# Kernel tuning notes

Measured on AMD Instinct MI355X. Metric: run time of the kernel, lower is better.

The kernel has to match this reference:

```python
import jax, jax.numpy as jnp
import numpy as np

N = 50000
E = 800000
D_IN = 128
H = 256
L = 3


def setup_inputs() -> dict:
    key = jax.random.key(0)
    ks = jax.random.split(key, 12)
    x = jax.random.normal(ks[0], (N, D_IN), dtype=jnp.float32)
    edge_index = jax.random.randint(ks[1], (2, E), 0, N, dtype=jnp.int32)
    edge_attr = jax.random.uniform(ks[2], (E, 4), dtype=jnp.float32)
    s_enc = 1.0 / np.sqrt(D_IN)
    s_h = 1.0 / np.sqrt(H)
    W_enc = jax.random.uniform(ks[3], (D_IN, H), minval=-s_enc, maxval=s_enc)
    b_enc = jax.random.uniform(ks[4], (H,), minval=-s_enc, maxval=s_enc)
    W_g = jax.random.uniform(ks[5], (L, H, H), minval=-s_h, maxval=s_h)
    b_g = jax.random.uniform(ks[6], (L, H), minval=-s_h, maxval=s_h)
    W_out = jax.random.uniform(ks[7], (H, H), minval=-s_h, maxval=s_h)
    b_out = jax.random.uniform(ks[8], (H,), minval=-s_h, maxval=s_h)
    return {"x": x, "edge_index": edge_index, "edge_attr": edge_attr,
            "W_enc": W_enc, "b_enc": b_enc, "W_g": W_g, "b_g": b_g,
            "W_out": W_out, "b_out": b_out}


def _gcn_norm(edge_index, n):
    # PyG GCNConv: add self-loops, symmetric normalization D^-1/2 (A+I) D^-1/2
    loops = jnp.arange(n, dtype=edge_index.dtype)
    src = jnp.concatenate([edge_index[0], loops])  # [E+N]
    dst = jnp.concatenate([edge_index[1], loops])  # [E+N]
    deg = jax.ops.segment_sum(jnp.ones_like(dst, dtype=jnp.float32), dst, num_segments=n)
    dinv = jnp.where(deg > 0, jax.lax.rsqrt(deg), 0.0)
    norm = dinv[src] * dinv[dst]  # [E+N]
    return src, dst, norm


def _gcn_conv(h, W, b, src, dst, norm, n):
    m = h @ W                                  # [N,H] transform first
    agg = jax.ops.segment_sum(m[src] * norm[:, None], dst, num_segments=n)
    return agg + b


def reference(x, edge_index, edge_attr, W_enc, b_enc, W_g, b_g, W_out, b_out):
    n = x.shape[0]
    src, dst, norm = _gcn_norm(edge_index, n)
    h = jax.nn.relu(x @ W_enc + b_enc)
    for i in range(W_g.shape[0]):
        h = jax.nn.relu(_gcn_conv(h, W_g[i], b_g[i], src, dst, norm, n))
        # dropout is identity in eval mode
    return h @ W_out + b_out
```

## Files before the change

### kernel.cpp

```cpp
#include <hip/hip_runtime.h>
#include <math.h>

#define N_NODES 50000
#define N_EDGES 800000
#define D_IN    128
#define H_DIM   256
#define L_LAYERS 3
#define SCAN_BLOCKS ((N_NODES + 255) / 256)

typedef _Float16 f16x8 __attribute__((ext_vector_type(8)));
typedef _Float16 f16x4 __attribute__((ext_vector_type(4)));
typedef float    f32x4 __attribute__((ext_vector_type(4)));


__global__ __launch_bounds__(256) void zero_kernel(int* __restrict__ counts,
                                                   int* __restrict__ cursor, int n) {
    int i = blockIdx.x * 256 + threadIdx.x;
    if (i < n) { counts[i] = 0; cursor[i] = 0; }
}

__global__ __launch_bounds__(256) void hist_kernel(const int* __restrict__ dst,
                                                   int* __restrict__ counts, int e_cnt) {
    int e = blockIdx.x * 256 + threadIdx.x;
    if (e < e_cnt) atomicAdd(&counts[dst[e]], 1);
}

__global__ __launch_bounds__(256) void scanA_kernel(const int* __restrict__ counts,
                                                    int* __restrict__ blocksum,
                                                    float* __restrict__ dinv, int n) {
    __shared__ int s[256];
    int t = threadIdx.x;
    int i = blockIdx.x * 256 + t;
    int v = (i < n) ? counts[i] : 0;
    if (i < n) dinv[i] = rsqrtf((float)(v + 1));
    s[t] = v;
    __syncthreads();
#pragma unroll
    for (int d = 128; d > 0; d >>= 1) {
        if (t < d) s[t] += s[t + d];
        __syncthreads();
    }
    if (t == 0) blocksum[blockIdx.x] = s[0];
}

__global__ __launch_bounds__(256) void scanB_kernel(int* __restrict__ blocksum,
                                                    int* __restrict__ offsets,
                                                    int nblocks, int n, int total) {
    __shared__ int s[256];
    int t = threadIdx.x;
    int v = (t < nblocks) ? blocksum[t] : 0;
    s[t] = v;
    __syncthreads();
#pragma unroll
    for (int d = 1; d < 256; d <<= 1) {
        int x = (t >= d) ? s[t - d] : 0;
        __syncthreads();
        s[t] += x;
        __syncthreads();
    }
    if (t < nblocks) blocksum[t] = s[t] - v;
    if (t == 0) offsets[n] = total;
}

__global__ __launch_bounds__(256) void scanC_kernel(const int* __restrict__ counts,
                                                    const int* __restrict__ blocksum,
                                                    int* __restrict__ offsets, int n) {
    __shared__ int s[256];
    int t = threadIdx.x;
    int i = blockIdx.x * 256 + t;
    int v = (i < n) ? counts[i] : 0;
    s[t] = v;
    __syncthreads();
#pragma unroll
    for (int d = 1; d < 256; d <<= 1) {
        int x = (t >= d) ? s[t - d] : 0;
        __syncthreads();
        s[t] += x;
        __syncthreads();
    }
    if (i < n) offsets[i] = blocksum[blockIdx.x] + s[t] - v;
}

__global__ __launch_bounds__(256) void fill_kernel(const int* __restrict__ src,
                                                   const int* __restrict__ dst,
                                                   const int* __restrict__ offsets,
                                                   int* __restrict__ cursor,
                                                   const float* __restrict__ dinv,
                                                   int* __restrict__ csr_src,
                                                   float* __restrict__ csr_w, int e_cnt) {
    int e = blockIdx.x * 256 + threadIdx.x;
    if (e < e_cnt) {
        int d = dst[e];
        int pos = offsets[d] + atomicAdd(&cursor[d], 1);
        int s = src[e];
        csr_src[pos] = s;
        csr_w[pos]   = dinv[s];
    }
}


__global__ __launch_bounds__(256) void aggregate_kernel(const _Float16* __restrict__ h,
                                                        const int* __restrict__ offsets,
                                                        const int* __restrict__ csr_src,
                                                        const float* __restrict__ csr_w,
                                                        const float* __restrict__ dinv,
                                                        _Float16* __restrict__ outp, int n) {
    int wave = threadIdx.x >> 6;
    int lane = threadIdx.x & 63;
    int v = blockIdx.x * 4 + wave;
    if (v >= n) return;
    int c = lane * 4;
    float dv = dinv[v];
    f16x4 self = *(const f16x4*)(h + (size_t)v * H_DIM + c);
    float ax = dv * (float)self[0];
    float ay = dv * (float)self[1];
    float az = dv * (float)self[2];
    float aw = dv * (float)self[3];

    int e  = offsets[v];
    int e1 = offsets[v + 1];

    for (; e + 15 < e1; e += 16) {
        int   s_[16]; float w_[16]; f16x4 r_[16];
#pragma unroll
        for (int j = 0; j < 16; ++j) { s_[j] = csr_src[e + j]; w_[j] = csr_w[e + j]; }
#pragma unroll
        for (int j = 0; j < 16; ++j) r_[j] = *(const f16x4*)(h + (size_t)s_[j] * H_DIM + c);
#pragma unroll
        for (int j = 0; j < 16; ++j) {
            ax += w_[j] * (float)r_[j][0];
            ay += w_[j] * (float)r_[j][1];
            az += w_[j] * (float)r_[j][2];
            aw += w_[j] * (float)r_[j][3];
        }
    }
    if (e + 7 < e1) {
        int   s_[8]; float w_[8]; f16x4 r_[8];
#pragma unroll
        for (int j = 0; j < 8; ++j) { s_[j] = csr_src[e + j]; w_[j] = csr_w[e + j]; }
#pragma unroll
        for (int j = 0; j < 8; ++j) r_[j] = *(const f16x4*)(h + (size_t)s_[j] * H_DIM + c);
#pragma unroll
        for (int j = 0; j < 8; ++j) {
            ax += w_[j] * (float)r_[j][0];
            ay += w_[j] * (float)r_[j][1];
            az += w_[j] * (float)r_[j][2];
            aw += w_[j] * (float)r_[j][3];
        }
        e += 8;
    }
    if (e + 3 < e1) {
        int   s_[4]; float w_[4]; f16x4 r_[4];
#pragma unroll
        for (int j = 0; j < 4; ++j) { s_[j] = csr_src[e + j]; w_[j] = csr_w[e + j]; }
#pragma unroll
        for (int j = 0; j < 4; ++j) r_[j] = *(const f16x4*)(h + (size_t)s_[j] * H_DIM + c);
#pragma unroll
        for (int j = 0; j < 4; ++j) {
            ax += w_[j] * (float)r_[j][0];
            ay += w_[j] * (float)r_[j][1];
            az += w_[j] * (float)r_[j][2];
            aw += w_[j] * (float)r_[j][3];
        }
        e += 4;
    }
    if (e + 1 < e1) {
        int   s0 = csr_src[e],  s1 = csr_src[e + 1];
        float w0 = csr_w[e],    w1 = csr_w[e + 1];
        f16x4 a = *(const f16x4*)(h + (size_t)s0 * H_DIM + c);
        f16x4 b = *(const f16x4*)(h + (size_t)s1 * H_DIM + c);
        ax += w0 * (float)a[0] + w1 * (float)b[0];
        ay += w0 * (float)a[1] + w1 * (float)b[1];
        az += w0 * (float)a[2] + w1 * (float)b[2];
        aw += w0 * (float)a[3] + w1 * (float)b[3];
        e += 2;
    }
    if (e < e1) {
        int   s0 = csr_src[e];
        float w0 = csr_w[e];
        f16x4 a = *(const f16x4*)(h + (size_t)s0 * H_DIM + c);
        ax += w0 * (float)a[0]; ay += w0 * (float)a[1];
        az += w0 * (float)a[2]; aw += w0 * (float)a[3];
    }
    f16x4 o;
    o[0] = (_Float16)(ax * dv);
    o[1] = (_Float16)(ay * dv);
    o[2] = (_Float16)(az * dv);
    o[3] = (_Float16)(aw * dv);
    *(f16x4*)(outp + (size_t)v * H_DIM + c) = o;
}


#define WCONV_TOTAL 294912

__global__ __launch_bounds__(256) void wconv_kernel(const float* __restrict__ W_enc,
                                                    const float* __restrict__ W_g,
                                                    const float* __restrict__ W_out,
                                                    _Float16* __restrict__ whi,
                                                    _Float16* __restrict__ wlo) {
    int gid = blockIdx.x * 256 + threadIdx.x;
    if (gid >= WCONV_TOTAL) return;
    const float* src; int base, e;
    if (gid < 32768)       { src = W_enc; base = 0;      e = gid; }
    else if (gid < 229376) { src = W_g;   base = 32768;  e = gid - 32768; }
    else                   { src = W_out; base = 229376; e = gid - 229376; }
    int k = e >> 8;
    int n = e & 255;
    float x = src[e];
    _Float16 hb = (_Float16)x;
    _Float16 lb = (_Float16)(x - (float)hb);
    int dst = base + (k >> 5) * 8192 + (n >> 4) * 512 + ((k & 31) >> 3) * 128
            + (n & 15) * 8 + (k & 7);
    whi[dst] = hb;
    wlo[dst] = lb;
}


template <int KC, int AMODE, int OUT16>
__global__ __launch_bounds__(256, 4) void mfma_gemm(const float* __restrict__ Af,
                                                    const _Float16* __restrict__ A16,
                                                    const _Float16* __restrict__ WhG,
                                                    const _Float16* __restrict__ WlG,
                                                    const float* __restrict__ bias,
                                                    float* __restrict__ Cf,
                                                    _Float16* __restrict__ Ch,
                                                    int n, int relu) {
    constexpr int K   = KC * 32;
    constexpr int PKC = (KC >= 8) ? 4 : KC;
    constexpr int NPH = KC / PKC;
    __shared__ _Float16 Wlds[PKC * 2 * 2048];

    int t = threadIdx.x;
    int w = t >> 6;
    int lane = t & 63;
    int q  = blockIdx.x >> 8;
    int rt = blockIdx.x & 255;
    if (rt * 256 >= n) return;
    int colbase = q * 64;
    int mrow = lane & 15;
    int koct = (lane >> 4) * 8;
    int rbase = rt * 256 + w * 64;

    int rows[4];
#pragma unroll
    for (int mt = 0; mt < 4; ++mt) {
        int r = rbase + mt * 16 + mrow;
        rows[mt] = (r < n) ? r : (n - 1);
    }

    f32x4 acc[4][4];
#pragma unroll
    for (int mt = 0; mt < 4; ++mt)
#pragma unroll
        for (int c = 0; c < 4; ++c)
            acc[mt][c] = (f32x4)(0.0f);

    f16x8 a16p[2][4];
    float4 af0[4], af1[4];
    if (AMODE == 1) {
#pragma unroll
        for (int mt = 0; mt < 4; ++mt) {
            a16p[0][mt] = *(const f16x8*)(A16 + (size_t)rows[mt] * K + koct);
            a16p[1][mt] = *(const f16x8*)(A16 + (size_t)rows[mt] * K + 32 + koct);
        }
    } else {
#pragma unroll
        for (int mt = 0; mt < 4; ++mt) {
            const float* p = Af + (size_t)rows[mt] * K + koct;
            af0[mt] = *(const float4*)p;
            af1[mt] = *(const float4*)(p + 4);
        }
    }

#pragma unroll
    for (int ph = 0; ph < NPH; ++ph) {
        if (ph) __syncthreads();
#pragma unroll
        for (int pk = 0; pk < PKC; ++pk) {
            int kc = ph * PKC + pk;
            __builtin_amdgcn_global_load_lds(
                (const __attribute__((address_space(1))) unsigned int*)(WhG + (size_t)kc * 8192 + q * 2048 + t * 8),
                (__attribute__((address_space(3))) unsigned int*)(&Wlds[(pk * 2 + 0) * 2048 + t * 8]), 16, 0, 0);
            __builtin_amdgcn_global_load_lds(
                (const __attribute__((address_space(1))) unsigned int*)(WlG + (size_t)kc * 8192 + q * 2048 + t * 8),
                (__attribute__((address_space(3))) unsigned int*)(&Wlds[(pk * 2 + 1) * 2048 + t * 8]), 16, 0, 0);
        }
        __syncthreads();

#pragma unroll
        for (int pk = 0; pk < PKC; ++pk) {
            int kc = ph * PKC + pk;
            f16x8 ah[4], al[4];
            if (AMODE == 0) {
#pragma unroll
                for (int mt = 0; mt < 4; ++mt) {
                    float4 c0 = af0[mt], c1 = af1[mt];
                    if (kc + 1 < KC) {
                        const float* p = Af + (size_t)rows[mt] * K + (kc + 1) * 32 + koct;
                        af0[mt] = *(const float4*)p;
                        af1[mt] = *(const float4*)(p + 4);
                    }
                    float xs[8] = {c0.x, c0.y, c0.z, c0.w, c1.x, c1.y, c1.z, c1.w};
                    f16x8 H, L;
#pragma unroll
                    for (int j = 0; j < 8; ++j) {
                        _Float16 hb = (_Float16)xs[j];
                        H[j] = hb;
                        L[j] = (_Float16)(xs[j] - (float)hb);
                    }
                    ah[mt] = H;
                    al[mt] = L;
                }
            }

#pragma unroll
            for (int c = 0; c < 4; ++c) {
                f16x8 bh = *(const f16x8*)&Wlds[(pk * 2 + 0) * 2048 + c * 512 + lane * 8];
                f16x8 bl = *(const f16x8*)&Wlds[(pk * 2 + 1) * 2048 + c * 512 + lane * 8];
#pragma unroll
                for (int mt = 0; mt < 4; ++mt) {
                    if (AMODE == 1) {
                        f16x8 a = a16p[kc & 1][mt];
                        acc[mt][c] = __builtin_amdgcn_mfma_f32_16x16x32_f16(a, bh, acc[mt][c], 0, 0, 0);
                        acc[mt][c] = __builtin_amdgcn_mfma_f32_16x16x32_f16(a, bl, acc[mt][c], 0, 0, 0);
                    } else {
                        acc[mt][c] = __builtin_amdgcn_mfma_f32_16x16x32_f16(ah[mt], bh, acc[mt][c], 0, 0, 0);
                        acc[mt][c] = __builtin_amdgcn_mfma_f32_16x16x32_f16(ah[mt], bl, acc[mt][c], 0, 0, 0);
                        acc[mt][c] = __builtin_amdgcn_mfma_f32_16x16x32_f16(al[mt], bh, acc[mt][c], 0, 0, 0);
                    }
                }
            }

            if (AMODE == 1 && kc + 2 < KC) {
#pragma unroll
                for (int mt = 0; mt < 4; ++mt)
                    a16p[kc & 1][mt] = *(const f16x8*)(A16 + (size_t)rows[mt] * K + (kc + 2) * 32 + koct);
            }
        }
    }

    int colq = lane & 15;
    int rowq = (lane >> 4) * 4;
#pragma unroll
    for (int c = 0; c < 4; ++c) {
        int col = colbase + c * 16 + colq;
        float b = bias[col];
#pragma unroll
        for (int mt = 0; mt < 4; ++mt) {
            int rb = rbase + mt * 16 + rowq;
#pragma unroll
            for (int r = 0; r < 4; ++r) {
                int row = rb + r;
                if (row < n) {
                    float v = acc[mt][c][r] + b;
                    if (relu) v = fmaxf(v, 0.f);
                    if (OUT16) Ch[(size_t)row * H_DIM + col] = (_Float16)v;
                    else       Cf[(size_t)row * H_DIM + col] = v;
                }
            }
        }
    }
}


extern "C" void kernel_launch(void* const* d_in, const int* in_sizes, int n_in,
                              void* d_out, int out_size, void* d_ws, size_t ws_size,
                              hipStream_t stream) {
    const float* x     = (const float*)d_in[0];
    const int*   ei    = (const int*)d_in[1];
    const float* W_enc = (const float*)d_in[3];
    const float* b_enc = (const float*)d_in[4];
    const float* W_g   = (const float*)d_in[5];
    const float* b_g   = (const float*)d_in[6];
    const float* W_out = (const float*)d_in[7];
    const float* b_out = (const float*)d_in[8];
    float* out = (float*)d_out;

    char* ws = (char*)d_ws;
    size_t off = 0;
    auto alloc = [&](size_t bytes) -> void* {
        void* p = ws + off;
        off = (off + bytes + 255) & ~(size_t)255;
        return p;
    };
    int*       counts   = (int*)alloc((size_t)N_NODES * 4);
    int*       offsets  = (int*)alloc((size_t)(N_NODES + 1) * 4);
    int*       cursor   = (int*)alloc((size_t)N_NODES * 4);
    float*     dinv     = (float*)alloc((size_t)N_NODES * 4);
    int*       blocksum = (int*)alloc((size_t)SCAN_BLOCKS * 4);
    int*       csr_src  = (int*)alloc((size_t)N_EDGES * 4);
    float*     csr_w    = (float*)alloc((size_t)N_EDGES * 4);
    _Float16*  h16      = (_Float16*)alloc((size_t)N_NODES * H_DIM * 2);
    _Float16*  agg16    = (_Float16*)alloc((size_t)N_NODES * H_DIM * 2);
    _Float16*  whi      = (_Float16*)alloc((size_t)WCONV_TOTAL * 2);
    _Float16*  wlo      = (_Float16*)alloc((size_t)WCONV_TOTAL * 2);

    const int* src = ei;
    const int* dst = ei + N_EDGES;

    zero_kernel<<<(N_NODES + 255) / 256, 256, 0, stream>>>(counts, cursor, N_NODES);
    hist_kernel<<<(N_EDGES + 255) / 256, 256, 0, stream>>>(dst, counts, N_EDGES);
    scanA_kernel<<<SCAN_BLOCKS, 256, 0, stream>>>(counts, blocksum, dinv, N_NODES);
    scanB_kernel<<<1, 256, 0, stream>>>(blocksum, offsets, SCAN_BLOCKS, N_NODES, N_EDGES);
    scanC_kernel<<<SCAN_BLOCKS, 256, 0, stream>>>(counts, blocksum, offsets, N_NODES);
    fill_kernel<<<(N_EDGES + 255) / 256, 256, 0, stream>>>(src, dst, offsets, cursor, dinv,
                                                           csr_src, csr_w, N_EDGES);
    wconv_kernel<<<(WCONV_TOTAL + 255) / 256, 256, 0, stream>>>(W_enc, W_g, W_out, whi, wlo);

    mfma_gemm<4, 0, 1><<<1024, 256, 0, stream>>>(x, (const _Float16*)nullptr,
                                                 whi, wlo, b_enc,
                                                 (float*)nullptr, h16, N_NODES, 1);
    for (int l = 0; l < L_LAYERS; ++l) {
        aggregate_kernel<<<N_NODES / 4, 256, 0, stream>>>(h16, offsets, csr_src, csr_w, dinv,
                                                          agg16, N_NODES);
        mfma_gemm<8, 1, 1><<<1024, 256, 0, stream>>>((const float*)nullptr, agg16,
                                                     whi + 32768 + (size_t)l * 65536,
                                                     wlo + 32768 + (size_t)l * 65536,
                                                     b_g + (size_t)l * H_DIM,
                                                     (float*)nullptr, h16, N_NODES, 1);
    }
    mfma_gemm<8, 1, 0><<<1024, 256, 0, stream>>>((const float*)nullptr, h16,
                                                 whi + 229376, wlo + 229376, b_out,
                                                 out, (_Float16*)nullptr, N_NODES, 0);
}
```

Baseline: 530.2 us.

## Pack CSR src/weight into int2 and split wave halves across edges with 16B loads

The CSR source index and edge weight are interleaved into a single int2 array, so the aggregate kernel fetches both with one load. Each wave now uses 32 lanes with 8-half (16-byte) vector loads per row, and the two half-waves take alternating edges. The partial sums are combined with a cross-half shuffle before the store. The aim is fewer, wider gather instructions and fewer index/weight loads per edge, at the cost of an extra shuffle reduction and idle half-lanes on odd tail edges.

Result: no change. 529.3 us (-0.2%).

```diff
diff --git a/kernel.cpp b/kernel.cpp
--- a/kernel.cpp
+++ b/kernel.cpp
@@ -81,113 +81,110 @@
     if (i < n) offsets[i] = blocksum[blockIdx.x] + s[t] - v;
 }
 
+
 __global__ __launch_bounds__(256) void fill_kernel(const int* __restrict__ src,
                                                    const int* __restrict__ dst,
                                                    const int* __restrict__ offsets,
                                                    int* __restrict__ cursor,
                                                    const float* __restrict__ dinv,
-                                                   int* __restrict__ csr_src,
-                                                   float* __restrict__ csr_w, int e_cnt) {
+                                                   int2* __restrict__ csr, int e_cnt) {
     int e = blockIdx.x * 256 + threadIdx.x;
     if (e < e_cnt) {
         int d = dst[e];
         int pos = offsets[d] + atomicAdd(&cursor[d], 1);
         int s = src[e];
-        csr_src[pos] = s;
-        csr_w[pos]   = dinv[s];
+        csr[pos] = make_int2(s, __float_as_int(dinv[s]));
     }
 }
 
 
 __global__ __launch_bounds__(256) void aggregate_kernel(const _Float16* __restrict__ h,
                                                         const int* __restrict__ offsets,
-                                                        const int* __restrict__ csr_src,
-                                                        const float* __restrict__ csr_w,
+                                                        const int2* __restrict__ csr,
                                                         const float* __restrict__ dinv,
                                                         _Float16* __restrict__ outp, int n) {
     int wave = threadIdx.x >> 6;
     int lane = threadIdx.x & 63;
     int v = blockIdx.x * 4 + wave;
     if (v >= n) return;
-    int c = lane * 4;
+    int hi  = lane >> 5;
+    int col = (lane & 31) * 8;
     float dv = dinv[v];
-    f16x4 self = *(const f16x4*)(h + (size_t)v * H_DIM + c);
-    float ax = dv * (float)self[0];
-    float ay = dv * (float)self[1];
-    float az = dv * (float)self[2];
-    float aw = dv * (float)self[3];
+
+    float acc[8];
+    f16x8 self = *(const f16x8*)(h + (size_t)v * H_DIM + col);
+#pragma unroll
+    for (int k = 0; k < 8; ++k) acc[k] = hi ? 0.0f : dv * (float)self[k];
 
     int e  = offsets[v];
     int e1 = offsets[v + 1];
 
     for (; e + 15 < e1; e += 16) {
-        int   s_[16]; float w_[16]; f16x4 r_[16];
-#pragma unroll
-        for (int j = 0; j < 16; ++j) { s_[j] = csr_src[e + j]; w_[j] = csr_w[e + j]; }
-#pragma unroll
-        for (int j = 0; j < 16; ++j) r_[j] = *(const f16x4*)(h + (size_t)s_[j] * H_DIM + c);
-#pragma unroll
-        for (int j = 0; j < 16; ++j) {
-            ax += w_[j] * (float)r_[j][0];
-            ay += w_[j] * (float)r_[j][1];
-            az += w_[j] * (float)r_[j][2];
-            aw += w_[j] * (float)r_[j][3];
+        int2 rec[8]; f16x8 r[8];
+#pragma unroll
+        for (int j = 0; j < 8; ++j) rec[j] = csr[e + 2 * j + hi];
+#pragma unroll
+        for (int j = 0; j < 8; ++j) r[j] = *(const f16x8*)(h + (size_t)rec[j].x * H_DIM + col);
+#pragma unroll
+        for (int j = 0; j < 8; ++j) {
+            float w = __int_as_float(rec[j].y);
+#pragma unroll
+            for (int k = 0; k < 8; ++k) acc[k] += w * (float)r[j][k];
         }
     }
     if (e + 7 < e1) {
-        int   s_[8]; float w_[8]; f16x4 r_[8];
-#pragma unroll
-        for (int j = 0; j < 8; ++j) { s_[j] = csr_src[e + j]; w_[j] = csr_w[e + j]; }
-#pragma unroll
-        for (int j = 0; j < 8; ++j) r_[j] = *(const f16x4*)(h + (size_t)s_[j] * H_DIM + c);
-#pragma unroll
-        for (int j = 0; j < 8; ++j) {
-            ax += w_[j] * (float)r_[j][0];
-            ay += w_[j] * (float)r_[j][1];
-            az += w_[j] * (float)r_[j][2];
-            aw += w_[j] * (float)r_[j][3];
+        int2 rec[4]; f16x8 r[4];
+#pragma unroll
+        for (int j = 0; j < 4; ++j) rec[j] = csr[e + 2 * j + hi];
+#pragma unroll
+        for (int j = 0; j < 4; ++j) r[j] = *(const f16x8*)(h + (size_t)rec[j].x * H_DIM + col);
+#pragma unroll
+        for (int j = 0; j < 4; ++j) {
+            float w = __int_as_float(rec[j].y);
+#pragma unroll
+            for (int k = 0; k < 8; ++k) acc[k] += w * (float)r[j][k];
         }
         e += 8;
     }
     if (e + 3 < e1) {
-        int   s_[4]; float w_[4]; f16x4 r_[4];
-#pragma unroll
-        for (int j = 0; j < 4; ++j) { s_[j] = csr_src[e + j]; w_[j] = csr_w[e + j]; }
-#pragma unroll
-        for (int j = 0; j < 4; ++j) r_[j] = *(const f16x4*)(h + (size_t)s_[j] * H_DIM + c);
-#pragma unroll
-        for (int j = 0; j < 4; ++j) {
-            ax += w_[j] * (float)r_[j][0];
-            ay += w_[j] * (float)r_[j][1];
-            az += w_[j] * (float)r_[j][2];
-            aw += w_[j] * (float)r_[j][3];
+        int2 rec[2]; f16x8 r[2];
+#pragma unroll
+        for (int j = 0; j < 2; ++j) rec[j] = csr[e + 2 * j + hi];
+#pragma unroll
+        for (int j = 0; j < 2; ++j) r[j] = *(const f16x8*)(h + (size_t)rec[j].x * H_DIM + col);
+#pragma unroll
+        for (int j = 0; j < 2; ++j) {
+            float w = __int_as_float(rec[j].y);
+#pragma unroll
+            for (int k = 0; k < 8; ++k) acc[k] += w * (float)r[j][k];
         }
         e += 4;
     }
     if (e + 1 < e1) {
-        int   s0 = csr_src[e],  s1 = csr_src[e + 1];
-        float w0 = csr_w[e],    w1 = csr_w[e + 1];
-        f16x4 a = *(const f16x4*)(h + (size_t)s0 * H_DIM + c);
-        f16x4 b = *(const f16x4*)(h + (size_t)s1 * H_DIM + c);
-        ax += w0 * (float)a[0] + w1 * (float)b[0];
-        ay += w0 * (float)a[1] + w1 * (float)b[1];
-        az += w0 * (float)a[2] + w1 * (float)b[2];
-        aw += w0 * (float)a[3] + w1 * (float)b[3];
+        int2 rec = csr[e + hi];
+        f16x8 r = *(const f16x8*)(h + (size_t)rec.x * H_DIM + col);
+        float w = __int_as_float(rec.y);
+#pragma unroll
+        for (int k = 0; k < 8; ++k) acc[k] += w * (float)r[k];
         e += 2;
     }
-    if (e < e1) {
-        int   s0 = csr_src[e];
-        float w0 = csr_w[e];
-        f16x4 a = *(const f16x4*)(h + (size_t)s0 * H_DIM + c);
-        ax += w0 * (float)a[0]; ay += w0 * (float)a[1];
-        az += w0 * (float)a[2]; aw += w0 * (float)a[3];
-    }
-    f16x4 o;
-    o[0] = (_Float16)(ax * dv);
-    o[1] = (_Float16)(ay * dv);
-    o[2] = (_Float16)(az * dv);
-    o[3] = (_Float16)(aw * dv);
-    *(f16x4*)(outp + (size_t)v * H_DIM + c) = o;
+    if (e < e1 && hi == 0) {
+        int2 rec = csr[e];
+        f16x8 r = *(const f16x8*)(h + (size_t)rec.x * H_DIM + col);
+        float w = __int_as_float(rec.y);
+#pragma unroll
+        for (int k = 0; k < 8; ++k) acc[k] += w * (float)r[k];
+    }
+
+#pragma unroll
+    for (int k = 0; k < 8; ++k) acc[k] += __shfl_xor(acc[k], 32, 64);
+
+    if (hi == 0) {
+        f16x8 o;
+#pragma unroll
+        for (int k = 0; k < 8; ++k) o[k] = (_Float16)(acc[k] * dv);
+        *(f16x8*)(outp + (size_t)v * H_DIM + col) = o;
+    }
 }
 
 
@@ -388,8 +385,7 @@
     int*       cursor   = (int*)alloc((size_t)N_NODES * 4);
     float*     dinv     = (float*)alloc((size_t)N_NODES * 4);
     int*       blocksum = (int*)alloc((size_t)SCAN_BLOCKS * 4);
-    int*       csr_src  = (int*)alloc((size_t)N_EDGES * 4);
-    float*     csr_w    = (float*)alloc((size_t)N_EDGES * 4);
+    int2*      csr      = (int2*)alloc((size_t)N_EDGES * 8);
     _Float16*  h16      = (_Float16*)alloc((size_t)N_NODES * H_DIM * 2);
     _Float16*  agg16    = (_Float16*)alloc((size_t)N_NODES * H_DIM * 2);
     _Float16*  whi      = (_Float16*)alloc((size_t)WCONV_TOTAL * 2);
@@ -404,14 +400,14 @@
     scanB_kernel<<<1, 256, 0, stream>>>(blocksum, offsets, SCAN_BLOCKS, N_NODES, N_EDGES);
     scanC_kernel<<<SCAN_BLOCKS, 256, 0, stream>>>(counts, blocksum, offsets, N_NODES);
     fill_kernel<<<(N_EDGES + 255) / 256, 256, 0, stream>>>(src, dst, offsets, cursor, dinv,
-                                                           csr_src, csr_w, N_EDGES);
+                                                           csr, N_EDGES);
     wconv_kernel<<<(WCONV_TOTAL + 255) / 256, 256, 0, stream>>>(W_enc, W_g, W_out, whi, wlo);
 
     mfma_gemm<4, 0, 1><<<1024, 256, 0, stream>>>(x, (const _Float16*)nullptr,
                                                  whi, wlo, b_enc,
                                                  (float*)nullptr, h16, N_NODES, 1);
     for (int l = 0; l < L_LAYERS; ++l) {
-        aggregate_kernel<<<N_NODES / 4, 256, 0, stream>>>(h16, offsets, csr_src, csr_w, dinv,
+        aggregate_kernel<<<N_NODES / 4, 256, 0, stream>>>(h16, offsets, csr, dinv,
                                                           agg16, N_NODES);
         mfma_gemm<8, 1, 1><<<1024, 256, 0, stream>>>((const float*)nullptr, agg16,
                                                      whi + 32768 + (size_t)l * 65536,
```
